# Optimization experiments

Hardware: AMD Instinct MI355X
Metric: run time of the kernel (lower is better)

The kernel has to match this reference:

```python
import jax, jax.numpy as jnp
import numpy as np

PD = 256            # pretrain_dim == dim_in (standard mode)
DZ = 128            # dim_z
PD2 = PD + 2        # feature dim after concatenating 2-d coords
FD = PD + 2 * PD2   # final_dim = 772
TEMP = float(DZ) ** 0.5
EPS = 1e-12
N1, N2 = 4096, 2048


def _lin_init(key, din, dout):
    w = jax.random.normal(key, (dout, din), jnp.float32) * 0.02
    b = jnp.zeros((dout,), jnp.float32)
    return w, b


def _lin(x, w, b):
    return x @ w.T + b


def setup_inputs() -> dict:
    key = jax.random.key(0)
    ks = jax.random.split(key, 13)
    lm_X = jax.random.normal(ks[0], (N1, PD), jnp.float32)
    lm_Y = jax.random.normal(ks[1], (N1, 2), jnp.float32)
    tg_X = jax.random.normal(ks[2], (N2, PD), jnp.float32)
    tg_Y = jax.random.normal(ks[3], (N2, 2), jnp.float32)
    lm_delay = jax.random.uniform(ks[4], (N1,), jnp.float32)
    tg_delay = jax.random.uniform(ks[5], (N2,), jnp.float32)
    aq_w, aq_b = _lin_init(ks[6], PD, DZ)    # att_attribute q proj
    ak_w, ak_b = _lin_init(ks[7], PD, DZ)    # att_attribute k proj
    w1_w, w1_b = _lin_init(ks[8], PD2, PD2)  # self.w_1
    w2_w, w2_b = _lin_init(ks[9], PD2, PD2)  # self.w_2
    pq_w, pq_b = _lin_init(ks[10], FD, DZ)   # pred attention q proj
    pk_w, pk_b = _lin_init(ks[11], PD, DZ)   # pred attention k proj
    pv_w, pv_b = _lin_init(ks[12], 2, 2)     # pred attention v proj
    gamma1 = jnp.ones((1, 1), jnp.float32)
    gamma2 = jnp.ones((1, 1), jnp.float32)
    gamma3 = jnp.ones((1, 1), jnp.float32)
    alpha = jnp.ones((1, 1), jnp.float32)
    beta = jnp.zeros((1, 1), jnp.float32)
    return dict(lm_X=lm_X, lm_Y=lm_Y, tg_X=tg_X, tg_Y=tg_Y,
                lm_delay=lm_delay, tg_delay=tg_delay,
                aq_w=aq_w, aq_b=aq_b, ak_w=ak_w, ak_b=ak_b,
                w1_w=w1_w, w1_b=w1_b, w2_w=w2_w, w2_b=w2_b,
                pq_w=pq_w, pq_b=pq_b, pk_w=pk_w, pk_b=pk_b,
                pv_w=pv_w, pv_b=pv_b,
                gamma1=gamma1, gamma2=gamma2, gamma3=gamma3,
                alpha=alpha, beta=beta)


def reference(lm_X, lm_Y, tg_X, tg_Y, lm_delay, tg_delay,
              aq_w, aq_b, ak_w, ak_b,
              w1_w, w1_b, w2_w, w2_b,
              pq_w, pq_b, pk_w, pk_b, pv_w, pv_b,
              gamma1, gamma2, gamma3, alpha, beta):
    n2 = tg_X.shape[0]
    a = alpha[0, 0]
    b0 = beta[0, 0]

    lm_feature = jnp.concatenate([lm_X, lm_Y], axis=1)            # [N1, PD2]
    tg_feature_0 = jnp.concatenate([tg_X, jnp.zeros((n2, 2), lm_X.dtype)], axis=1)
    router_0 = jnp.mean(lm_feature, axis=0)                        # [PD2]

    delay_score = jnp.exp(-gamma1[0, 0] * (a * lm_delay + b0))     # [N1]
    rou0 = jnp.exp(-gamma2[0, 0] * (a * tg_delay + b0))            # [N2]
    rou1 = jnp.exp(-gamma3[0, 0] * (a * tg_delay + b0))            # [N2]

    # SimpleAttention1: attribute score of targets over landmarks
    q = _lin(tg_X, aq_w, aq_b)
    k = _lin(lm_X, ak_w, ak_b)
    attr = jnp.exp(jax.nn.softmax((q / TEMP) @ k.T, axis=-1))      # [N2, N1]

    # Degree-normalized propagation of adj_matrix_0 (block-structured:
    # lm rows = identity, tg rows = [attr | I | rou0-col], router row = [delay | 0 | 1]).
    deg_tg0 = 1.0 + attr.sum(axis=1) + rou0                        # [N2]
    tg_prop0 = (attr @ lm_feature + tg_feature_0 + rou0[:, None] * router_0[None, :]) \
               / (deg_tg0 + EPS)[:, None]
    router_prop0 = (delay_score @ lm_feature + router_0) / (1.0 + delay_score.sum() + EPS)

    tg_feature_1 = _lin(tg_prop0, w1_w, w1_b)                      # [N2, PD2]
    router_1 = _lin(router_prop0[None, :], w1_w, w1_b)             # [1, PD2]

    # Second propagation: adj_matrix_1 = I + rou1 on tg->router column.
    tg_prop1 = (tg_feature_1 + rou1[:, None] * router_1) / (1.0 + rou1 + EPS)[:, None]
    tg_feature_2 = _lin(tg_prop1, w2_w, w2_b)                      # [N2, PD2]

    final_tg_feature = jnp.concatenate([tg_X, tg_feature_1, tg_feature_2], axis=-1)  # [N2, FD]

    # SimpleAttention2 (collaborative MLP prediction)
    q2 = _lin(final_tg_feature, pq_w, pq_b)
    k2 = _lin(lm_X, pk_w, pk_b)
    v2 = _lin(lm_Y, pv_w, pv_b)
    attn2 = jax.nn.softmax((q2 / TEMP) @ k2.T, axis=-1)            # [N2, N1]
    y_pred = attn2 @ v2                                            # [N2, 2]
    return y_pred, final_tg_feature
```

## Files before the change

### kernel.cpp

```cpp
#include <hip/hip_runtime.h>

#define N1 4096
#define N2 2048
#define PD 256
#define DZ 128
#define PD2 258
#define PD2P 264
#define FD 772
#define FDP 776
#define APN 272
#define APLD 72
#define SPLITS 16

typedef short s8v __attribute__((ext_vector_type(8)));
typedef float f32x4 __attribute__((ext_vector_type(4)));

__device__ __forceinline__ short f2b(float f) {
    union { float f; unsigned u; } v; v.f = f;
    unsigned r = v.u + 0x7fffu + ((v.u >> 16) & 1u);
    return (short)(r >> 16);
}
__device__ __forceinline__ float sb2f(short s) {
    union { unsigned u; float f; } v;
    v.u = ((unsigned)(unsigned short)s) << 16;
    return v.f;
}

constexpr int S0 = N1 * PD;
constexpr int S1 = S0 + N2 * PD;
constexpr int S2 = S1 + DZ * PD;
constexpr int S3 = S2 + 256 * 256;
constexpr int S4 = S3 + DZ * FDP;
constexpr int S5 = S4 + PD2 * PD2P;
constexpr int S6 = S5 + PD2 * PD2P;
constexpr int S7 = S6 + APN * N1;
constexpr int S8 = S7 + N1;
constexpr int S9 = S8 + 2048 + 8192 + 12288 + 256;

__global__ __launch_bounds__(256) void cvt_all(
    const float* __restrict__ lmX, const float* __restrict__ lmY,
    const float* __restrict__ tgX,
    const float* __restrict__ aqw, const float* __restrict__ akw,
    const float* __restrict__ pkw, const float* __restrict__ pqw,
    const float* __restrict__ w1w, const float* __restrict__ w2w,
    const float* __restrict__ lmd, const float* __restrict__ tgd,
    const float* __restrict__ g1, const float* __restrict__ g2,
    const float* __restrict__ g3, const float* __restrict__ al,
    const float* __restrict__ be,
    const float* __restrict__ pvw, const float* __restrict__ pvb,
    const float* __restrict__ akb, const float* __restrict__ pkb,
    short* __restrict__ lmXb, short* __restrict__ tgXb,
    short* __restrict__ aqwb, short* __restrict__ wkkb,
    short* __restrict__ pqwb,
    short* __restrict__ w1wb, short* __restrict__ w2wb,
    short* __restrict__ lmFTb,
    float* __restrict__ dscore, float* __restrict__ rou0,
    float* __restrict__ rou1, float* __restrict__ v2b,
    float* __restrict__ Z, short* __restrict__ finalFb,
    short* __restrict__ tgp1b, float* __restrict__ biasKK,
    float* __restrict__ outF)
{
    int i = blockIdx.x * 256 + threadIdx.x;
    if (i < S0) { lmXb[i] = f2b(lmX[i]); return; }
    if (i < S1) { int j = i - S0; int r = j >> 8, c = j & 255;
                  float v = tgX[j];
                  tgXb[j] = f2b(v);
                  outF[(size_t)r * FD + c] = v;
                  finalFb[(size_t)r * FDP + c] = f2b(v); return; }
    if (i < S2) { int j = i - S1; aqwb[j] = f2b(aqw[j]); return; }
    if (i < S3) { int j = i - S2; int r = j >> 8, c = j & 255;
                  wkkb[j] = f2b(r < 128 ? akw[r * 256 + c] : pkw[(r - 128) * 256 + c]);
                  return; }
    if (i < S4) { int j = i - S3; int r = j / FDP, c = j - r * FDP;
                  pqwb[j] = (c < FD) ? f2b(pqw[r * FD + c]) : (short)0; return; }
    if (i < S5) { int j = i - S4; int r = j / PD2P, c = j - r * PD2P;
                  w1wb[j] = (c < PD2) ? f2b(w1w[r * PD2 + c]) : (short)0; return; }
    if (i < S6) { int j = i - S5; int r = j / PD2P, c = j - r * PD2P;
                  w2wb[j] = (c < PD2) ? f2b(w2w[r * PD2 + c]) : (short)0; return; }
    if (i < S7) { int j = i - S6; int c = j >> 12, r = j & (N1 - 1);
                  float v = 0.f;
                  if (c < PD) v = lmX[r * PD + c];
                  else if (c < PD2) v = lmY[r * 2 + (c - PD)];
                  else if (c == PD2) v = 1.0f;
                  lmFTb[j] = f2b(v); return; }
    if (i < S8) { int j = i - S7;
                  float a = al[0], b = be[0];
                  dscore[j] = __expf(-g1[0] * (a * lmd[j] + b));
                  float y0 = lmY[2 * j], y1 = lmY[2 * j + 1];
                  v2b[2 * j]     = pvw[0] * y0 + pvw[1] * y1 + pvb[0];
                  v2b[2 * j + 1] = pvw[2] * y0 + pvw[3] * y1 + pvb[1];
                  if (j < N2) { float t = a * tgd[j] + b;
                                rou0[j] = __expf(-g2[0] * t);
                                rou1[j] = __expf(-g3[0] * t); }
                  return; }
    if (i < S9) { int j = i - S8;
                  if (j < 2048) { Z[j] = 0.f; return; }
                  j -= 2048;
                  if (j < 8192) { int r = j >> 2, c = FD + (j & 3);
                                  finalFb[(size_t)r * FDP + c] = 0; return; }
                  j -= 8192;
                  if (j < 12288) { int r = j / 6, c = PD2 + (j - r * 6);
                                   tgp1b[(size_t)r * PD2P + c] = 0; return; }
                  j -= 12288;
                  biasKK[j] = (j < 128) ? akb[j] : pkb[j - 128];
                  return; }
}

__global__ __launch_bounds__(256) void router_kernel(const short* __restrict__ lmFTb,
                                                     const float* __restrict__ dscore,
                                                     float* __restrict__ router0,
                                                     float* __restrict__ routerp0) {
    int c = blockIdx.x;
    const short* rowp = lmFTb + (size_t)c * N1;
    __shared__ float r1[256], r2[256], r3[256];
    int tid = threadIdx.x;
    float s1 = 0.f, s2 = 0.f, s3 = 0.f;
    for (int i = tid; i < N1; i += 256) {
        float v = sb2f(rowp[i]);
        float d = dscore[i];
        s1 += v; s2 += d * v; s3 += d;
    }
    r1[tid] = s1; r2[tid] = s2; r3[tid] = s3; __syncthreads();
    for (int o = 128; o > 0; o >>= 1) {
        if (tid < o) { r1[tid] += r1[tid + o]; r2[tid] += r2[tid + o]; r3[tid] += r3[tid + o]; }
        __syncthreads();
    }
    if (tid == 0) {
        float r0 = r1[0] / (float)N1;
        router0[c] = r0;
        routerp0[c] = (r2[0] + r0) / (1.f + r3[0] + 1e-12f);
    }
}

__global__ __launch_bounds__(256) void router1_kernel(const float* __restrict__ rp0,
                                                      const float* __restrict__ w1w,
                                                      const float* __restrict__ w1b,
                                                      float* __restrict__ router1) {
    for (int c = threadIdx.x; c < PD2; c += 256) {
        float s = w1b[c];
        const float* wr = w1w + (size_t)c * PD2;
        for (int k = 0; k < PD2; ++k) s += rp0[k] * wr[k];
        router1[c] = s;
    }
}

__global__ __launch_bounds__(256) void proj_gemm(
    const short* __restrict__ A, const short* __restrict__ B,
    const float* __restrict__ bias, short* __restrict__ outB,
    int M, int N, int KP, int ldo, float scale)
{
    __shared__ short Als[64][40];
    __shared__ short Bls[64][40];
    const int tid = threadIdx.x;
    const int wave = tid >> 6, lane = tid & 63;
    const int wm = wave >> 1, wn = wave & 1;
    const int lm = lane & 15, lq = lane >> 4;
    const int row0 = blockIdx.y * 64, col0 = blockIdx.x * 64;
    f32x4 acc[2][2];
    const f32x4 zero4 = {0.f, 0.f, 0.f, 0.f};
#pragma unroll
    for (int mt = 0; mt < 2; ++mt)
#pragma unroll
        for (int nt = 0; nt < 2; ++nt) acc[mt][nt] = zero4;
    const s8v zero8 = {0, 0, 0, 0, 0, 0, 0, 0};
    for (int k0 = 0; k0 < KP; k0 += 32) {
        {
            int r = tid >> 2, cg = tid & 3;
            int gk = k0 + cg * 8;
            s8v va = zero8, vb = zero8;
            if (row0 + r < M && gk < KP) va = *(const s8v*)(A + (size_t)(row0 + r) * KP + gk);
            if (col0 + r < N && gk < KP) vb = *(const s8v*)(B + (size_t)(col0 + r) * KP + gk);
            *(s8v*)(&Als[r][cg * 8]) = va;
            *(s8v*)(&Bls[r][cg * 8]) = vb;
        }
        __syncthreads();
        s8v af[2], bf[2];
#pragma unroll
        for (int mt = 0; mt < 2; ++mt)
            af[mt] = *(const s8v*)(&Als[wm * 32 + mt * 16 + lm][lq * 8]);
#pragma unroll
        for (int nt = 0; nt < 2; ++nt)
            bf[nt] = *(const s8v*)(&Bls[wn * 32 + nt * 16 + lm][lq * 8]);
#pragma unroll
        for (int mt = 0; mt < 2; ++mt)
#pragma unroll
            for (int nt = 0; nt < 2; ++nt)
                acc[mt][nt] = __builtin_amdgcn_mfma_f32_16x16x32_bf16(
                    af[mt], bf[nt], acc[mt][nt], 0, 0, 0);
        __syncthreads();
    }
#pragma unroll
    for (int mt = 0; mt < 2; ++mt)
#pragma unroll
        for (int nt = 0; nt < 2; ++nt) {
            int c = col0 + wn * 32 + nt * 16 + lm;
            if (c >= N) continue;
            float bv = bias ? bias[c] : 0.f;
#pragma unroll
            for (int i = 0; i < 4; ++i) {
                int r = row0 + wm * 32 + mt * 16 + lq * 4 + i;
                if (r >= M) continue;
                outB[(size_t)r * ldo + c] = f2b(scale * (acc[mt][nt][i] + bv));
            }
        }
}

__global__ __launch_bounds__(256) void scores_e(
    const short* __restrict__ Q,
    const short* __restrict__ Kk,
    short* __restrict__ E, float* __restrict__ Z)
{
    __shared__ short Als[128][40];
    __shared__ short Bls[128][40];
    const int tid = threadIdx.x;
    const int wave = tid >> 6, lane = tid & 63;
    const int wm = wave >> 1, wn = wave & 1;
    const int lm = lane & 15, lq = lane >> 4;
    const int row0 = blockIdx.y * 128, col0 = blockIdx.x * 128;
    f32x4 acc[4][4];
    const f32x4 zero4 = {0.f, 0.f, 0.f, 0.f};
#pragma unroll
    for (int mt = 0; mt < 4; ++mt)
#pragma unroll
        for (int nt = 0; nt < 4; ++nt) acc[mt][nt] = zero4;
    for (int k0 = 0; k0 < 128; k0 += 32) {
#pragma unroll
        for (int l = 0; l < 2; ++l) {
            int id = l * 256 + tid;
            int r = id >> 2, cg = id & 3;
            int gk = k0 + cg * 8;
            *(s8v*)(&Als[r][cg * 8]) = *(const s8v*)(Q + (size_t)(row0 + r) * DZ + gk);
            *(s8v*)(&Bls[r][cg * 8]) = *(const s8v*)(Kk + (size_t)(col0 + r) * 256 + gk);
        }
        __syncthreads();
        s8v af[4], bf[4];
#pragma unroll
        for (int mt = 0; mt < 4; ++mt)
            af[mt] = *(const s8v*)(&Als[wm * 64 + mt * 16 + lm][lq * 8]);
#pragma unroll
        for (int nt = 0; nt < 4; ++nt)
            bf[nt] = *(const s8v*)(&Bls[wn * 64 + nt * 16 + lm][lq * 8]);
#pragma unroll
        for (int mt = 0; mt < 4; ++mt)
#pragma unroll
            for (int nt = 0; nt < 4; ++nt)
                acc[mt][nt] = __builtin_amdgcn_mfma_f32_16x16x32_bf16(
                    af[mt], bf[nt], acc[mt][nt], 0, 0, 0);
        __syncthreads();
    }
#pragma unroll
    for (int mt = 0; mt < 4; ++mt)
#pragma unroll
        for (int i = 0; i < 4; ++i) {
            int r = row0 + wm * 64 + mt * 16 + lq * 4 + i;
            float rs = 0.f;
#pragma unroll
            for (int nt = 0; nt < 4; ++nt) {
                int c = col0 + wn * 64 + nt * 16 + lm;
                float e = __expf(acc[mt][nt][i]);
                E[(size_t)r * N1 + c] = f2b(e);
                rs += e;
            }
#pragma unroll
            for (int msk = 1; msk < 16; msk <<= 1) rs += __shfl_xor(rs, msk, 64);
            if (lm == 0) atomicAdd(&Z[r], rs);
        }
}

__global__ __launch_bounds__(256) void ap_gemm(const short* __restrict__ E,
                                               const float* __restrict__ Z,
                                               const short* __restrict__ lmFTb,
                                               float* __restrict__ part)
{
    __shared__ short Als[128 * APLD];
    __shared__ short Bls[APN * APLD];
    const int tid = threadIdx.x;
    const int wave = tid >> 6, lane = tid & 63;
    const int lm = lane & 15, lq = lane >> 4;
    const int s = blockIdx.x;
    const int row0 = blockIdx.y * 128;
    const int kbase = s * (N1 / SPLITS);
    f32x4 acc0[17], acc1[17];
    const f32x4 zero4 = {0.f, 0.f, 0.f, 0.f};
#pragma unroll
    for (int nt = 0; nt < 17; ++nt) { acc0[nt] = zero4; acc1[nt] = zero4; }

    for (int it = 0; it < (N1 / SPLITS) / 64; ++it) {
        int k0 = kbase + it * 64;
#pragma unroll
        for (int l = 0; l < 4; ++l) {
            int id = l * 256 + tid;
            int r = id >> 3, g = id & 7;
            s8v ev = *(const s8v*)(E + (size_t)(row0 + r) * N1 + k0 + g * 8);
            float invZ = __builtin_amdgcn_rcpf(Z[row0 + r]);
            s8v av;
#pragma unroll
            for (int j = 0; j < 8; ++j)
                av[j] = f2b(__expf(sb2f(ev[j]) * invZ));
            *(s8v*)(&Als[r * APLD + g * 8]) = av;
        }
#pragma unroll
        for (int l = 0; l < 9; ++l) {
            int id = l * 256 + tid;
            if (id < APN * 8) {
                int r = id >> 3, g = id & 7;
                *(s8v*)(&Bls[r * APLD + g * 8]) =
                    *(const s8v*)(lmFTb + (size_t)r * N1 + k0 + g * 8);
            }
        }
        __syncthreads();
        s8v a00 = *(const s8v*)(&Als[(wave * 32 + lm) * APLD + lq * 8]);
        s8v a01 = *(const s8v*)(&Als[(wave * 32 + lm) * APLD + 32 + lq * 8]);
        s8v a10 = *(const s8v*)(&Als[(wave * 32 + 16 + lm) * APLD + lq * 8]);
        s8v a11 = *(const s8v*)(&Als[(wave * 32 + 16 + lm) * APLD + 32 + lq * 8]);
#pragma unroll
        for (int nt = 0; nt < 17; ++nt) {
            s8v b0 = *(const s8v*)(&Bls[(nt * 16 + lm) * APLD + lq * 8]);
            s8v b1 = *(const s8v*)(&Bls[(nt * 16 + lm) * APLD + 32 + lq * 8]);
            acc0[nt] = __builtin_amdgcn_mfma_f32_16x16x32_bf16(a00, b0, acc0[nt], 0, 0, 0);
            acc0[nt] = __builtin_amdgcn_mfma_f32_16x16x32_bf16(a01, b1, acc0[nt], 0, 0, 0);
            acc1[nt] = __builtin_amdgcn_mfma_f32_16x16x32_bf16(a10, b0, acc1[nt], 0, 0, 0);
            acc1[nt] = __builtin_amdgcn_mfma_f32_16x16x32_bf16(a11, b1, acc1[nt], 0, 0, 0);
        }
        __syncthreads();
    }
    float* op = part + (size_t)s * N2 * APN;
#pragma unroll
    for (int nt = 0; nt < 17; ++nt) {
        int c = nt * 16 + lm;
#pragma unroll
        for (int i = 0; i < 4; ++i) {
            int r = row0 + wave * 32 + lq * 4 + i;
            op[(size_t)r * APN + c] = acc0[nt][i];
            op[(size_t)(r + 16) * APN + c] = acc1[nt][i];
        }
    }
}

__global__ __launch_bounds__(256) void fix_tgp0(const float* __restrict__ part,
                                                const float* __restrict__ tgX,
                                                const float* __restrict__ rou0,
                                                const float* __restrict__ router0,
                                                short* __restrict__ outb) {
    int r = blockIdx.x;
    int tid = threadIdx.x;
    __shared__ float sAsum;
    float s0 = 0.f, s1 = 0.f;
#pragma unroll
    for (int s = 0; s < SPLITS; ++s)
        s0 += part[((size_t)s * N2 + r) * APN + tid];
    if (tid < 8) {
#pragma unroll
        for (int s = 0; s < SPLITS; ++s)
            s1 += part[((size_t)s * N2 + r) * APN + 256 + tid];
    }
    if (tid == 2) sAsum = s1;
    __syncthreads();
    float ro = rou0[r];
    float inv = 1.f / (1.f + sAsum + ro + 1e-12f);
    {
        float v = (s0 + tgX[(size_t)r * PD + tid] + ro * router0[tid]) * inv;
        outb[(size_t)r * PD2P + tid] = f2b(v);
    }
    if (tid < 8) {
        int c = 256 + tid;
        float v = 0.f;
        if (c < PD2) v = (s1 + ro * router0[c]) * inv;
        outb[(size_t)r * PD2P + c] = f2b(v);
    }
}

__global__ __launch_bounds__(256) void w_gemm(
    const short* __restrict__ A, const short* __restrict__ B,
    const float* __restrict__ bias,
    float* __restrict__ outFcol, short* __restrict__ fFbcol,
    const float* __restrict__ rou1, const float* __restrict__ router1,
    short* __restrict__ tgp1b)
{
    __shared__ short Als[64][40];
    __shared__ short Bls[64][40];
    const int tid = threadIdx.x;
    const int wave = tid >> 6, lane = tid & 63;
    const int wm = wave >> 1, wn = wave & 1;
    const int lm = lane & 15, lq = lane >> 4;
    const int row0 = blockIdx.y * 64, col0 = blockIdx.x * 64;
    f32x4 acc[2][2];
    const f32x4 zero4 = {0.f, 0.f, 0.f, 0.f};
#pragma unroll
    for (int mt = 0; mt < 2; ++mt)
#pragma unroll
        for (int nt = 0; nt < 2; ++nt) acc[mt][nt] = zero4;
    const s8v zero8 = {0, 0, 0, 0, 0, 0, 0, 0};
    for (int k0 = 0; k0 < PD2P; k0 += 32) {
        {
            int r = tid >> 2, cg = tid & 3;
            int gk = k0 + cg * 8;
            s8v va = zero8, vb = zero8;
            if (gk < PD2P) {
                va = *(const s8v*)(A + (size_t)(row0 + r) * PD2P + gk);
                if (col0 + r < PD2) vb = *(const s8v*)(B + (size_t)(col0 + r) * PD2P + gk);
            }
            *(s8v*)(&Als[r][cg * 8]) = va;
            *(s8v*)(&Bls[r][cg * 8]) = vb;
        }
        __syncthreads();
        s8v af[2], bf[2];
#pragma unroll
        for (int mt = 0; mt < 2; ++mt)
            af[mt] = *(const s8v*)(&Als[wm * 32 + mt * 16 + lm][lq * 8]);
#pragma unroll
        for (int nt = 0; nt < 2; ++nt)
            bf[nt] = *(const s8v*)(&Bls[wn * 32 + nt * 16 + lm][lq * 8]);
#pragma unroll
        for (int mt = 0; mt < 2; ++mt)
#pragma unroll
            for (int nt = 0; nt < 2; ++nt)
                acc[mt][nt] = __builtin_amdgcn_mfma_f32_16x16x32_bf16(
                    af[mt], bf[nt], acc[mt][nt], 0, 0, 0);
        __syncthreads();
    }
#pragma unroll
    for (int mt = 0; mt < 2; ++mt)
#pragma unroll
        for (int nt = 0; nt < 2; ++nt) {
            int c = col0 + wn * 32 + nt * 16 + lm;
            if (c >= PD2) continue;
            float bv = bias[c];
            float rc = router1 ? router1[c] : 0.f;
#pragma unroll
            for (int i = 0; i < 4; ++i) {
                int r = row0 + wm * 32 + mt * 16 + lq * 4 + i;
                float v = acc[mt][nt][i] + bv;
                outFcol[(size_t)r * FD + c] = v;
                fFbcol[(size_t)r * FDP + c] = f2b(v);
                if (tgp1b) {
                    float ro = rou1[r];
                    float t = (v + ro * rc) / (1.f + ro + 1e-12f);
                    tgp1b[(size_t)r * PD2P + c] = f2b(t);
                }
            }
        }
}

__global__ __launch_bounds__(256) void attn2_flash(
    const short* __restrict__ Q,
    const short* __restrict__ Kk,
    const float* __restrict__ V, float* __restrict__ part2)
{
    __shared__ short Qls[64 * 136];
    __shared__ short Kls[64 * 136];
    __shared__ float Vls[128];
    const int tid = threadIdx.x;
    const int wave = tid >> 6, lane = tid & 63;
    const int lm = lane & 15, lq = lane >> 4;
    const int chunk = blockIdx.x;
    const int row0 = blockIdx.y * 64;
#pragma unroll
    for (int l = 0; l < 4; ++l) {
        int id = l * 256 + tid;
        int r = id >> 4, g = id & 15;
        *(s8v*)(&Qls[r * 136 + g * 8]) = *(const s8v*)(Q + (size_t)(row0 + r) * DZ + g * 8);
    }
    __syncthreads();
    s8v af[4];
#pragma unroll
    for (int ks = 0; ks < 4; ++ks)
        af[ks] = *(const s8v*)(&Qls[(wave * 16 + lm) * 136 + ks * 32 + lq * 8]);
    float z[4] = {0.f, 0.f, 0.f, 0.f}, y0[4] = {0.f, 0.f, 0.f, 0.f}, y1[4] = {0.f, 0.f, 0.f, 0.f};

    for (int t = 0; t < 8; ++t) {
        int col0 = chunk * 512 + t * 64;
        __syncthreads();
#pragma unroll
        for (int l = 0; l < 4; ++l) {
            int id = l * 256 + tid;
            int r = id >> 4, g = id & 15;
            *(s8v*)(&Kls[r * 136 + g * 8]) =
                *(const s8v*)(Kk + (size_t)(col0 + r) * 256 + 128 + g * 8);
        }
        if (tid < 128) Vls[tid] = V[col0 * 2 + tid];
        __syncthreads();
        f32x4 acc[4];
        const f32x4 zero4 = {0.f, 0.f, 0.f, 0.f};
#pragma unroll
        for (int nt = 0; nt < 4; ++nt) acc[nt] = zero4;
#pragma unroll
        for (int nt = 0; nt < 4; ++nt)
#pragma unroll
            for (int ks = 0; ks < 4; ++ks) {
                s8v bf = *(const s8v*)(&Kls[(nt * 16 + lm) * 136 + ks * 32 + lq * 8]);
                acc[nt] = __builtin_amdgcn_mfma_f32_16x16x32_bf16(af[ks], bf, acc[nt], 0, 0, 0);
            }
        float v0[4], v1[4];
#pragma unroll
        for (int nt = 0; nt < 4; ++nt) {
            v0[nt] = Vls[(nt * 16 + lm) * 2];
            v1[nt] = Vls[(nt * 16 + lm) * 2 + 1];
        }
#pragma unroll
        for (int i = 0; i < 4; ++i) {
            float e0 = __expf(acc[0][i]), e1 = __expf(acc[1][i]);
            float e2 = __expf(acc[2][i]), e3 = __expf(acc[3][i]);
            float pz = e0 + e1 + e2 + e3;
            float py0 = e0 * v0[0] + e1 * v0[1] + e2 * v0[2] + e3 * v0[3];
            float py1 = e0 * v1[0] + e1 * v1[1] + e2 * v1[2] + e3 * v1[3];
#pragma unroll
            for (int msk = 1; msk < 16; msk <<= 1) {
                pz  += __shfl_xor(pz, msk, 64);
                py0 += __shfl_xor(py0, msk, 64);
                py1 += __shfl_xor(py1, msk, 64);
            }
            z[i] += pz; y0[i] += py0; y1[i] += py1;
        }
    }
    if (lm == 0) {
#pragma unroll
        for (int i = 0; i < 4; ++i) {
            int r = row0 + wave * 16 + lq * 4 + i;
            float* p = part2 + ((size_t)r * 8 + chunk) * 4;
            p[0] = z[i]; p[1] = y0[i]; p[2] = y1[i];
        }
    }
}

__global__ void attn2_combine(const float* __restrict__ part2, float* __restrict__ out) {
    int r = blockIdx.x * blockDim.x + threadIdx.x;
    if (r >= N2) return;
    const float* p = part2 + (size_t)r * 32;
    float Zt = 0.f, Y0 = 0.f, Y1 = 0.f;
#pragma unroll
    for (int c = 0; c < 8; ++c) {
        Zt += p[c * 4]; Y0 += p[c * 4 + 1]; Y1 += p[c * 4 + 2];
    }
    out[2 * r] = Y0 / Zt;
    out[2 * r + 1] = Y1 / Zt;
}

extern "C" void kernel_launch(void* const* d_in, const int* in_sizes, int n_in,
                              void* d_out, int out_size, void* d_ws, size_t ws_size,
                              hipStream_t stream) {
    const float* lm_X = (const float*)d_in[0];
    const float* lm_Y = (const float*)d_in[1];
    const float* tg_X = (const float*)d_in[2];
    const float* lm_delay = (const float*)d_in[4];
    const float* tg_delay = (const float*)d_in[5];
    const float* aq_w = (const float*)d_in[6];
    const float* aq_b = (const float*)d_in[7];
    const float* ak_w = (const float*)d_in[8];
    const float* ak_b = (const float*)d_in[9];
    const float* w1_w = (const float*)d_in[10];
    const float* w1_b = (const float*)d_in[11];
    const float* w2_w = (const float*)d_in[12];
    const float* w2_b = (const float*)d_in[13];
    const float* pq_w = (const float*)d_in[14];
    const float* pq_b = (const float*)d_in[15];
    const float* pk_w = (const float*)d_in[16];
    const float* pk_b = (const float*)d_in[17];
    const float* pv_w = (const float*)d_in[18];
    const float* pv_b = (const float*)d_in[19];
    const float* g1 = (const float*)d_in[20];
    const float* g2 = (const float*)d_in[21];
    const float* g3 = (const float*)d_in[22];
    const float* al = (const float*)d_in[23];
    const float* be = (const float*)d_in[24];

    float* out = (float*)d_out;
    float* outF = out + (size_t)N2 * 2;

    char* base = (char*)d_ws;
    size_t off = 0;
    auto allocF = [&](size_t n) -> float* {
        float* p = (float*)(base + off);
        off += (n * 4 + 255) / 256 * 256;
        return p;
    };
    auto allocS = [&](size_t n) -> short* {
        short* p = (short*)(base + off);
        off += (n * 2 + 255) / 256 * 256;
        return p;
    };

    short* E        = allocS((size_t)N2 * N1);
    float* appart   = allocF((size_t)SPLITS * N2 * APN);
    short* lmFTb    = allocS((size_t)APN * N1);
    short* lmXb     = allocS((size_t)N1 * PD);
    short* tgXb     = allocS((size_t)N2 * PD);
    short* qb_b     = allocS((size_t)N2 * DZ);
    short* kk       = allocS((size_t)N1 * 256);
    short* q2_b     = allocS((size_t)N2 * DZ);
    short* tgp0b    = allocS((size_t)N2 * PD2P);
    short* tgp1b    = allocS((size_t)N2 * PD2P);
    short* finalFb  = allocS((size_t)N2 * FDP);
    short* aqwb     = allocS((size_t)DZ * PD);
    short* wkkb     = allocS((size_t)256 * 256);
    short* pqwb     = allocS((size_t)DZ * FDP);
    short* w1wb     = allocS((size_t)PD2 * PD2P);
    short* w2wb     = allocS((size_t)PD2 * PD2P);
    float* v2b      = allocF((size_t)N1 * 2);
    float* part2    = allocF((size_t)N2 * 32);
    float* Zbuf     = allocF(N2);
    float* biasKK   = allocF(256);
    float* router0  = allocF(PD2);
    float* routerp0 = allocF(PD2);
    float* router1  = allocF(PD2);
    float* dscore   = allocF(N1);
    float* rou0     = allocF(N2);
    float* rou1     = allocF(N2);

    const float INV_TEMP = 0.08838834764831845f;

    hipLaunchKernelGGL(cvt_all, dim3((S9 + 255) / 256), dim3(256), 0, stream,
                       lm_X, lm_Y, tg_X, aq_w, ak_w, pk_w, pq_w, w1_w, w2_w,
                       lm_delay, tg_delay, g1, g2, g3, al, be, pv_w, pv_b, ak_b, pk_b,
                       lmXb, tgXb, aqwb, wkkb, pqwb, w1wb, w2wb, lmFTb,
                       dscore, rou0, rou1, v2b, Zbuf, finalFb, tgp1b, biasKK, outF);
    hipLaunchKernelGGL(router_kernel, dim3(PD2), dim3(256), 0, stream,
                       lmFTb, dscore, router0, routerp0);
    hipLaunchKernelGGL(router1_kernel, dim3(1), dim3(256), 0, stream,
                       routerp0, w1_w, w1_b, router1);

    hipLaunchKernelGGL(proj_gemm, dim3(4, 64), dim3(256), 0, stream,
                       lmXb, wkkb, biasKK, kk, N1, 256, PD, 256, 1.f);
    hipLaunchKernelGGL(proj_gemm, dim3(2, 32), dim3(256), 0, stream,
                       tgXb, aqwb, aq_b, qb_b, N2, DZ, PD, DZ, INV_TEMP);
    hipLaunchKernelGGL(scores_e, dim3(32, 16), dim3(256), 0, stream, qb_b, kk, E, Zbuf);
    hipLaunchKernelGGL(ap_gemm, dim3(SPLITS, N2 / 128), dim3(256), 0, stream,
                       E, Zbuf, lmFTb, appart);
    hipLaunchKernelGGL(fix_tgp0, dim3(N2), dim3(256), 0, stream,
                       appart, tg_X, rou0, router0, tgp0b);
    hipLaunchKernelGGL(w_gemm, dim3(5, 32), dim3(256), 0, stream,
                       tgp0b, w1wb, w1_b, outF + 256, finalFb + 256, rou1, router1, tgp1b);
    hipLaunchKernelGGL(w_gemm, dim3(5, 32), dim3(256), 0, stream,
                       tgp1b, w2wb, w2_b, outF + 514, finalFb + 514,
                       nullptr, nullptr, nullptr);
    hipLaunchKernelGGL(proj_gemm, dim3(2, 32), dim3(256), 0, stream,
                       finalFb, pqwb, pq_b, q2_b, N2, DZ, FDP, DZ, INV_TEMP);
    hipLaunchKernelGGL(attn2_flash, dim3(8, N2 / 64), dim3(256), 0, stream,
                       q2_b, kk, v2b, part2);
    hipLaunchKernelGGL(attn2_combine, dim3((N2 + 255) / 256), dim3(256), 0, stream,
                       part2, out);
}
```

Measured before the change: 252.2 us.

## Fuse all stages into one persistent megakernel with grid-wide barriers

```diff
diff --git a/kernel.cpp b/kernel.cpp
--- a/kernel.cpp
+++ b/kernel.cpp
@@ -26,617 +26,626 @@
     return v.f;
 }
 
-constexpr int S0 = N1 * PD;
-constexpr int S1 = S0 + N2 * PD;
-constexpr int S2 = S1 + DZ * PD;
-constexpr int S3 = S2 + 256 * 256;
-constexpr int S4 = S3 + DZ * FDP;
-constexpr int S5 = S4 + PD2 * PD2P;
-constexpr int S6 = S5 + PD2 * PD2P;
-constexpr int S7 = S6 + APN * N1;
-constexpr int S8 = S7 + N1;
-constexpr int S9 = S8 + 2048 + 8192 + 12288 + 256;
-
-__global__ __launch_bounds__(256) void cvt_all(
-    const float* __restrict__ lmX, const float* __restrict__ lmY,
-    const float* __restrict__ tgX,
-    const float* __restrict__ aqw, const float* __restrict__ akw,
-    const float* __restrict__ pkw, const float* __restrict__ pqw,
-    const float* __restrict__ w1w, const float* __restrict__ w2w,
-    const float* __restrict__ lmd, const float* __restrict__ tgd,
-    const float* __restrict__ g1, const float* __restrict__ g2,
-    const float* __restrict__ g3, const float* __restrict__ al,
-    const float* __restrict__ be,
-    const float* __restrict__ pvw, const float* __restrict__ pvb,
-    const float* __restrict__ akb, const float* __restrict__ pkb,
-    short* __restrict__ lmXb, short* __restrict__ tgXb,
-    short* __restrict__ aqwb, short* __restrict__ wkkb,
-    short* __restrict__ pqwb,
-    short* __restrict__ w1wb, short* __restrict__ w2wb,
-    short* __restrict__ lmFTb,
-    float* __restrict__ dscore, float* __restrict__ rou0,
-    float* __restrict__ rou1, float* __restrict__ v2b,
-    float* __restrict__ Z, short* __restrict__ finalFb,
-    short* __restrict__ tgp1b, float* __restrict__ biasKK,
-    float* __restrict__ outF)
-{
-    int i = blockIdx.x * 256 + threadIdx.x;
-    if (i < S0) { lmXb[i] = f2b(lmX[i]); return; }
-    if (i < S1) { int j = i - S0; int r = j >> 8, c = j & 255;
-                  float v = tgX[j];
-                  tgXb[j] = f2b(v);
-                  outF[(size_t)r * FD + c] = v;
-                  finalFb[(size_t)r * FDP + c] = f2b(v); return; }
-    if (i < S2) { int j = i - S1; aqwb[j] = f2b(aqw[j]); return; }
-    if (i < S3) { int j = i - S2; int r = j >> 8, c = j & 255;
-                  wkkb[j] = f2b(r < 128 ? akw[r * 256 + c] : pkw[(r - 128) * 256 + c]);
-                  return; }
-    if (i < S4) { int j = i - S3; int r = j / FDP, c = j - r * FDP;
-                  pqwb[j] = (c < FD) ? f2b(pqw[r * FD + c]) : (short)0; return; }
-    if (i < S5) { int j = i - S4; int r = j / PD2P, c = j - r * PD2P;
-                  w1wb[j] = (c < PD2) ? f2b(w1w[r * PD2 + c]) : (short)0; return; }
-    if (i < S6) { int j = i - S5; int r = j / PD2P, c = j - r * PD2P;
-                  w2wb[j] = (c < PD2) ? f2b(w2w[r * PD2 + c]) : (short)0; return; }
-    if (i < S7) { int j = i - S6; int c = j >> 12, r = j & (N1 - 1);
-                  float v = 0.f;
-                  if (c < PD) v = lmX[r * PD + c];
-                  else if (c < PD2) v = lmY[r * 2 + (c - PD)];
-                  else if (c == PD2) v = 1.0f;
-                  lmFTb[j] = f2b(v); return; }
-    if (i < S8) { int j = i - S7;
-                  float a = al[0], b = be[0];
-                  dscore[j] = __expf(-g1[0] * (a * lmd[j] + b));
-                  float y0 = lmY[2 * j], y1 = lmY[2 * j + 1];
-                  v2b[2 * j]     = pvw[0] * y0 + pvw[1] * y1 + pvb[0];
-                  v2b[2 * j + 1] = pvw[2] * y0 + pvw[3] * y1 + pvb[1];
-                  if (j < N2) { float t = a * tgd[j] + b;
-                                rou0[j] = __expf(-g2[0] * t);
-                                rou1[j] = __expf(-g3[0] * t); }
-                  return; }
-    if (i < S9) { int j = i - S8;
-                  if (j < 2048) { Z[j] = 0.f; return; }
-                  j -= 2048;
-                  if (j < 8192) { int r = j >> 2, c = FD + (j & 3);
-                                  finalFb[(size_t)r * FDP + c] = 0; return; }
-                  j -= 8192;
-                  if (j < 12288) { int r = j / 6, c = PD2 + (j - r * 6);
-                                   tgp1b[(size_t)r * PD2P + c] = 0; return; }
-                  j -= 12288;
-                  biasKK[j] = (j < 128) ? akb[j] : pkb[j - 128];
-                  return; }
+struct P {
+    const float *lmX, *lmY, *tgX, *lmd, *tgd;
+    const float *aqw, *aqb, *akw, *akb, *w1w, *w1b, *w2w, *w2b;
+    const float *pqw, *pqb, *pkw, *pkb, *pvw, *pvb;
+    const float *g1, *g2, *g3, *al, *be;
+    short *lmFTb, *qb, *kk, *q2, *tgp0b, *tgp1b, *finalFb, *w1wb, *w2wb, *pqwb, *E;
+    float *appart, *v2b, *part2, *Z;
+    float *router0, *routerp0, *router1, *dscore, *rou0, *rou1;
+    float *out, *outF;
+    unsigned *bar;
+};
+
+__device__ __forceinline__ void gbar(unsigned* cnt, unsigned target) {
+    __syncthreads();
+    if (threadIdx.x == 0) {
+        __threadfence();
+        atomicAdd(cnt, 1u);
+        while (__hip_atomic_load(cnt, __ATOMIC_RELAXED, __HIP_MEMORY_SCOPE_AGENT) < target)
+            __builtin_amdgcn_s_sleep(2);
+        __threadfence();
+    }
+    __syncthreads();
 }
 
-__global__ __launch_bounds__(256) void router_kernel(const short* __restrict__ lmFTb,
-                                                     const float* __restrict__ dscore,
-                                                     float* __restrict__ router0,
-                                                     float* __restrict__ routerp0) {
-    int c = blockIdx.x;
-    const short* rowp = lmFTb + (size_t)c * N1;
-    __shared__ float r1[256], r2[256], r3[256];
-    int tid = threadIdx.x;
-    float s1 = 0.f, s2 = 0.f, s3 = 0.f;
-    for (int i = tid; i < N1; i += 256) {
-        float v = sb2f(rowp[i]);
-        float d = dscore[i];
-        s1 += v; s2 += d * v; s3 += d;
-    }
-    r1[tid] = s1; r2[tid] = s2; r3[tid] = s3; __syncthreads();
-    for (int o = 128; o > 0; o >>= 1) {
-        if (tid < o) { r1[tid] += r1[tid + o]; r2[tid] += r2[tid + o]; r3[tid] += r3[tid + o]; }
-        __syncthreads();
-    }
-    if (tid == 0) {
-        float r0 = r1[0] / (float)N1;
-        router0[c] = r0;
-        routerp0[c] = (r2[0] + r0) / (1.f + r3[0] + 1e-12f);
-    }
+#define F_TGX   (N2 * PD)
+#define F_W     (PD2 * PD2P)
+#define F_PQ    (DZ * FDP)
+#define F_DEL   4096
+#define F_Z     2048
+#define F_FPAD  (N2 * 4)
+#define F_TPAD  (N2 * 6)
+#define FT_TOT  (F_TGX + 2 * F_W + F_PQ + F_DEL + F_Z + F_FPAD + F_TPAD)
+
+__device__ __forceinline__ void mfma64(const short* Als, const short* Bls,
+                                       f32x4 acc[2][2], int wm, int wn, int lm, int lq) {
+    s8v af[2], bf[2];
+#pragma unroll
+    for (int mt = 0; mt < 2; ++mt)
+        af[mt] = *(const s8v*)(Als + (wm * 32 + mt * 16 + lm) * 40 + lq * 8);
+#pragma unroll
+    for (int nt = 0; nt < 2; ++nt)
+        bf[nt] = *(const s8v*)(Bls + (wn * 32 + nt * 16 + lm) * 40 + lq * 8);
+#pragma unroll
+    for (int mt = 0; mt < 2; ++mt)
+#pragma unroll
+        for (int nt = 0; nt < 2; ++nt)
+            acc[mt][nt] = __builtin_amdgcn_mfma_f32_16x16x32_bf16(
+                af[mt], bf[nt], acc[mt][nt], 0, 0, 0);
 }
 
-__global__ __launch_bounds__(256) void router1_kernel(const float* __restrict__ rp0,
-                                                      const float* __restrict__ w1w,
-                                                      const float* __restrict__ w1b,
-                                                      float* __restrict__ router1) {
-    for (int c = threadIdx.x; c < PD2; c += 256) {
-        float s = w1b[c];
-        const float* wr = w1w + (size_t)c * PD2;
-        for (int k = 0; k < PD2; ++k) s += rp0[k] * wr[k];
-        router1[c] = s;
-    }
-}
-
-__global__ __launch_bounds__(256) void proj_gemm(
-    const short* __restrict__ A, const short* __restrict__ B,
-    const float* __restrict__ bias, short* __restrict__ outB,
-    int M, int N, int KP, int ldo, float scale)
-{
-    __shared__ short Als[64][40];
-    __shared__ short Bls[64][40];
-    const int tid = threadIdx.x;
+__global__ __launch_bounds__(256) void mega(P p) {
+    __shared__ __align__(16) short LDS[28800];
+    const int bid = blockIdx.x, tid = threadIdx.x;
     const int wave = tid >> 6, lane = tid & 63;
     const int wm = wave >> 1, wn = wave & 1;
     const int lm = lane & 15, lq = lane >> 4;
-    const int row0 = blockIdx.y * 64, col0 = blockIdx.x * 64;
-    f32x4 acc[2][2];
     const f32x4 zero4 = {0.f, 0.f, 0.f, 0.f};
-#pragma unroll
-    for (int mt = 0; mt < 2; ++mt)
-#pragma unroll
-        for (int nt = 0; nt < 2; ++nt) acc[mt][nt] = zero4;
-    const s8v zero8 = {0, 0, 0, 0, 0, 0, 0, 0};
-    for (int k0 = 0; k0 < KP; k0 += 32) {
-        {
-            int r = tid >> 2, cg = tid & 3;
-            int gk = k0 + cg * 8;
+
+    for (int j = bid; j < 320; j += 256) {
+        int rt = j / 5, ct = j - rt * 5;
+        int r0 = rt * 64, c0 = ct * 64;
+        __syncthreads();
+#pragma unroll
+        for (int l = 0; l < 16; ++l) {
+            int idx = l * 256 + tid;
+            int i = idx >> 6, jj = idx & 63;
+            int c = c0 + jj;
+            float v = 0.f;
+            if (c < PD) v = p.lmX[(size_t)(r0 + i) * PD + c];
+            else if (c < PD2) v = p.lmY[(size_t)(r0 + i) * 2 + (c - PD)];
+            else if (c == PD2) v = 1.f;
+            LDS[jj * 65 + i] = f2b(v);
+        }
+        __syncthreads();
+#pragma unroll
+        for (int l = 0; l < 16; ++l) {
+            int idx = l * 256 + tid;
+            int cc = idx >> 6, i = idx & 63;
+            if (c0 + cc < APN)
+                p.lmFTb[(size_t)(c0 + cc) * N1 + r0 + i] = LDS[cc * 65 + i];
+        }
+    }
+    for (int i0 = bid * 256 + tid; i0 < FT_TOT; i0 += 65536) {
+        int j = i0;
+        if (j < F_TGX) {
+            int r = j >> 8, c = j & 255;
+            float v = p.tgX[j];
+            p.outF[(size_t)r * FD + c] = v;
+            p.finalFb[(size_t)r * FDP + c] = f2b(v);
+            continue;
+        }
+        j -= F_TGX;
+        if (j < F_W) { int r = j / PD2P, c = j - r * PD2P;
+            p.w1wb[j] = (c < PD2) ? f2b(p.w1w[r * PD2 + c]) : (short)0; continue; }
+        j -= F_W;
+        if (j < F_W) { int r = j / PD2P, c = j - r * PD2P;
+            p.w2wb[j] = (c < PD2) ? f2b(p.w2w[r * PD2 + c]) : (short)0; continue; }
+        j -= F_W;
+        if (j < F_PQ) { int r = j / FDP, c = j - r * FDP;
+            p.pqwb[j] = (c < FD) ? f2b(p.pqw[r * FD + c]) : (short)0; continue; }
+        j -= F_PQ;
+        if (j < F_DEL) {
+            float a = p.al[0], b = p.be[0];
+            p.dscore[j] = __expf(-p.g1[0] * (a * p.lmd[j] + b));
+            float y0 = p.lmY[2 * j], y1 = p.lmY[2 * j + 1];
+            p.v2b[2 * j]     = p.pvw[0] * y0 + p.pvw[1] * y1 + p.pvb[0];
+            p.v2b[2 * j + 1] = p.pvw[2] * y0 + p.pvw[3] * y1 + p.pvb[1];
+            if (j < N2) {
+                float t = a * p.tgd[j] + b;
+                p.rou0[j] = __expf(-p.g2[0] * t);
+                p.rou1[j] = __expf(-p.g3[0] * t);
+            }
+            continue;
+        }
+        j -= F_DEL;
+        if (j < F_Z) { p.Z[j] = 0.f; continue; }
+        j -= F_Z;
+        if (j < F_FPAD) { int r = j >> 2;
+            p.finalFb[(size_t)r * FDP + FD + (j & 3)] = 0; continue; }
+        j -= F_FPAD;
+        { int r = j / 6; p.tgp1b[(size_t)r * PD2P + PD2 + (j - r * 6)] = 0; }
+    }
+    gbar(p.bar, 256u * 1);
+
+    for (int j = bid; j < 578; j += 256) {
+        __syncthreads();
+        if (j < 258) {
+            float* r1 = (float*)LDS;
+            float* r2 = r1 + 256;
+            float* r3 = r2 + 256;
+            const short* rowp = p.lmFTb + (size_t)j * N1;
+            float s1 = 0.f, s2 = 0.f, s3 = 0.f;
+            for (int i = tid; i < N1; i += 256) {
+                float v = sb2f(rowp[i]);
+                float d = p.dscore[i];
+                s1 += v; s2 += d * v; s3 += d;
+            }
+            r1[tid] = s1; r2[tid] = s2; r3[tid] = s3; __syncthreads();
+            for (int o = 128; o > 0; o >>= 1) {
+                if (tid < o) { r1[tid] += r1[tid + o]; r2[tid] += r2[tid + o]; r3[tid] += r3[tid + o]; }
+                __syncthreads();
+            }
+            if (tid == 0) {
+                float r0v = r1[0] / (float)N1;
+                p.router0[j] = r0v;
+                p.routerp0[j] = (r2[0] + r0v) / (1.f + r3[0] + 1e-12f);
+            }
+        } else if (j < 514) {
+            int jt = j - 258;
+            int row0 = (jt >> 2) * 64, col0 = (jt & 3) * 64;
+            short* Als = LDS;
+            short* Bls = LDS + 64 * 40;
+            f32x4 acc[2][2] = {{zero4, zero4}, {zero4, zero4}};
+            int r = tid >> 2, cgp = tid & 3;
+            for (int k0 = 0; k0 < 256; k0 += 32) {
+                int gk = k0 + cgp * 8;
+                const float* ap = p.lmX + (size_t)(row0 + r) * PD + gk;
+                int c = col0 + r;
+                const float* bp = (c < 128) ? p.akw + (size_t)c * PD + gk
+                                            : p.pkw + (size_t)(c - 128) * PD + gk;
+                s8v va, vb;
+#pragma unroll
+                for (int q = 0; q < 8; ++q) { va[q] = f2b(ap[q]); vb[q] = f2b(bp[q]); }
+                *(s8v*)(Als + r * 40 + cgp * 8) = va;
+                *(s8v*)(Bls + r * 40 + cgp * 8) = vb;
+                __syncthreads();
+                mfma64(Als, Bls, acc, wm, wn, lm, lq);
+                __syncthreads();
+            }
+#pragma unroll
+            for (int mt = 0; mt < 2; ++mt)
+#pragma unroll
+                for (int nt = 0; nt < 2; ++nt) {
+                    int c = col0 + wn * 32 + nt * 16 + lm;
+                    float bv = (c < 128) ? p.akb[c] : p.pkb[c - 128];
+#pragma unroll
+                    for (int i = 0; i < 4; ++i) {
+                        int rr = row0 + wm * 32 + mt * 16 + lq * 4 + i;
+                        p.kk[(size_t)rr * 256 + c] = f2b(acc[mt][nt][i] + bv);
+                    }
+                }
+        } else {
+            int jt = j - 514;
+            int row0 = (jt >> 1) * 64, col0 = (jt & 1) * 64;
+            short* Als = LDS;
+            short* Bls = LDS + 64 * 40;
+            f32x4 acc[2][2] = {{zero4, zero4}, {zero4, zero4}};
+            int r = tid >> 2, cgp = tid & 3;
+            for (int k0 = 0; k0 < 256; k0 += 32) {
+                int gk = k0 + cgp * 8;
+                const float* ap = p.tgX + (size_t)(row0 + r) * PD + gk;
+                const float* bp = p.aqw + (size_t)(col0 + r) * PD + gk;
+                s8v va, vb;
+#pragma unroll
+                for (int q = 0; q < 8; ++q) { va[q] = f2b(ap[q]); vb[q] = f2b(bp[q]); }
+                *(s8v*)(Als + r * 40 + cgp * 8) = va;
+                *(s8v*)(Bls + r * 40 + cgp * 8) = vb;
+                __syncthreads();
+                mfma64(Als, Bls, acc, wm, wn, lm, lq);
+                __syncthreads();
+            }
+            const float INV_TEMP = 0.08838834764831845f;
+#pragma unroll
+            for (int mt = 0; mt < 2; ++mt)
+#pragma unroll
+                for (int nt = 0; nt < 2; ++nt) {
+                    int c = col0 + wn * 32 + nt * 16 + lm;
+                    float bv = p.aqb[c];
+#pragma unroll
+                    for (int i = 0; i < 4; ++i) {
+                        int rr = row0 + wm * 32 + mt * 16 + lq * 4 + i;
+                        p.qb[(size_t)rr * DZ + c] = f2b(INV_TEMP * (acc[mt][nt][i] + bv));
+                    }
+                }
+        }
+    }
+    gbar(p.bar, 256u * 2);
+
+    for (int j = bid; j < 513; j += 256) {
+        __syncthreads();
+        if (j < 512) {
+            int row0 = (j >> 5) * 128, col0 = (j & 31) * 128;
+            short* Als = LDS;
+            short* Bls = LDS + 128 * 40;
+            f32x4 acc[4][4];
+#pragma unroll
+            for (int mt = 0; mt < 4; ++mt)
+#pragma unroll
+                for (int nt = 0; nt < 4; ++nt) acc[mt][nt] = zero4;
+            for (int k0 = 0; k0 < 128; k0 += 32) {
+#pragma unroll
+                for (int l = 0; l < 2; ++l) {
+                    int id = l * 256 + tid;
+                    int r = id >> 2, cgp = id & 3;
+                    int gk = k0 + cgp * 8;
+                    *(s8v*)(Als + r * 40 + cgp * 8) =
+                        *(const s8v*)(p.qb + (size_t)(row0 + r) * DZ + gk);
+                    *(s8v*)(Bls + r * 40 + cgp * 8) =
+                        *(const s8v*)(p.kk + (size_t)(col0 + r) * 256 + gk);
+                }
+                __syncthreads();
+                s8v af[4], bf[4];
+#pragma unroll
+                for (int mt = 0; mt < 4; ++mt)
+                    af[mt] = *(const s8v*)(Als + (wm * 64 + mt * 16 + lm) * 40 + lq * 8);
+#pragma unroll
+                for (int nt = 0; nt < 4; ++nt)
+                    bf[nt] = *(const s8v*)(Bls + (wn * 64 + nt * 16 + lm) * 40 + lq * 8);
+#pragma unroll
+                for (int mt = 0; mt < 4; ++mt)
+#pragma unroll
+                    for (int nt = 0; nt < 4; ++nt)
+                        acc[mt][nt] = __builtin_amdgcn_mfma_f32_16x16x32_bf16(
+                            af[mt], bf[nt], acc[mt][nt], 0, 0, 0);
+                __syncthreads();
+            }
+#pragma unroll
+            for (int mt = 0; mt < 4; ++mt)
+#pragma unroll
+                for (int i = 0; i < 4; ++i) {
+                    int r = row0 + wm * 64 + mt * 16 + lq * 4 + i;
+                    float rs = 0.f;
+#pragma unroll
+                    for (int nt = 0; nt < 4; ++nt) {
+                        int c = col0 + wn * 64 + nt * 16 + lm;
+                        float e = __expf(acc[mt][nt][i]);
+                        p.E[(size_t)r * N1 + c] = f2b(e);
+                        rs += e;
+                    }
+#pragma unroll
+                    for (int msk = 1; msk < 16; msk <<= 1) rs += __shfl_xor(rs, msk, 64);
+                    if (lm == 0) atomicAdd(&p.Z[r], rs);
+                }
+        } else {
+            for (int c = tid; c < PD2; c += 256) {
+                float s = p.w1b[c];
+                const float* wr = p.w1w + (size_t)c * PD2;
+                for (int k = 0; k < PD2; ++k) s += p.routerp0[k] * wr[k];
+                p.router1[c] = s;
+            }
+        }
+    }
+    gbar(p.bar, 256u * 3);
+
+    {
+        int s = bid & 15, row0 = (bid >> 4) * 128;
+        int kbase = s * (N1 / SPLITS);
+        short* Als = LDS;
+        short* Bls = LDS + 128 * APLD;
+        f32x4 acc0[17], acc1[17];
+#pragma unroll
+        for (int nt = 0; nt < 17; ++nt) { acc0[nt] = zero4; acc1[nt] = zero4; }
+        for (int it = 0; it < (N1 / SPLITS) / 64; ++it) {
+            int k0 = kbase + it * 64;
+#pragma unroll
+            for (int l = 0; l < 4; ++l) {
+                int id = l * 256 + tid;
+                int r = id >> 3, g = id & 7;
+                s8v ev = *(const s8v*)(p.E + (size_t)(row0 + r) * N1 + k0 + g * 8);
+                float invZ = __builtin_amdgcn_rcpf(p.Z[row0 + r]);
+                s8v av;
+#pragma unroll
+                for (int q = 0; q < 8; ++q)
+                    av[q] = f2b(__expf(sb2f(ev[q]) * invZ));
+                *(s8v*)(Als + r * APLD + g * 8) = av;
+            }
+#pragma unroll
+            for (int l = 0; l < 9; ++l) {
+                int id = l * 256 + tid;
+                if (id < APN * 8) {
+                    int r = id >> 3, g = id & 7;
+                    *(s8v*)(Bls + r * APLD + g * 8) =
+                        *(const s8v*)(p.lmFTb + (size_t)r * N1 + k0 + g * 8);
+                }
+            }
+            __syncthreads();
+            s8v a00 = *(const s8v*)(Als + (wave * 32 + lm) * APLD + lq * 8);
+            s8v a01 = *(const s8v*)(Als + (wave * 32 + lm) * APLD + 32 + lq * 8);
+            s8v a10 = *(const s8v*)(Als + (wave * 32 + 16 + lm) * APLD + lq * 8);
+            s8v a11 = *(const s8v*)(Als + (wave * 32 + 16 + lm) * APLD + 32 + lq * 8);
+#pragma unroll
+            for (int nt = 0; nt < 17; ++nt) {
+                s8v b0 = *(const s8v*)(Bls + (nt * 16 + lm) * APLD + lq * 8);
+                s8v b1 = *(const s8v*)(Bls + (nt * 16 + lm) * APLD + 32 + lq * 8);
+                acc0[nt] = __builtin_amdgcn_mfma_f32_16x16x32_bf16(a00, b0, acc0[nt], 0, 0, 0);
+                acc0[nt] = __builtin_amdgcn_mfma_f32_16x16x32_bf16(a01, b1, acc0[nt], 0, 0, 0);
+                acc1[nt] = __builtin_amdgcn_mfma_f32_16x16x32_bf16(a10, b0, acc1[nt], 0, 0, 0);
+                acc1[nt] = __builtin_amdgcn_mfma_f32_16x16x32_bf16(a11, b1, acc1[nt], 0, 0, 0);
+            }
+            __syncthreads();
+        }
+        float* op = p.appart + (size_t)s * N2 * APN;
+#pragma unroll
+        for (int nt = 0; nt < 17; ++nt) {
+            int c = nt * 16 + lm;
+#pragma unroll
+            for (int i = 0; i < 4; ++i) {
+                int r = row0 + wave * 32 + lq * 4 + i;
+                op[(size_t)r * APN + c] = acc0[nt][i];
+                op[(size_t)(r + 16) * APN + c] = acc1[nt][i];
+            }
+        }
+    }
+    gbar(p.bar, 256u * 4);
+
+    for (int rr = 0; rr < 8; ++rr) {
+        int r = bid * 8 + rr;
+        float s0 = 0.f, s1 = 0.f;
+#pragma unroll
+        for (int s = 0; s < SPLITS; ++s)
+            s0 += p.appart[((size_t)s * N2 + r) * APN + tid];
+        if (tid < 8) {
+#pragma unroll
+            for (int s = 0; s < SPLITS; ++s)
+                s1 += p.appart[((size_t)s * N2 + r) * APN + 256 + tid];
+        }
+        __syncthreads();
+        if (tid == 2) *(float*)LDS = s1;
+        __syncthreads();
+        float asum = *(float*)LDS;
+        float ro = p.rou0[r];
+        float inv = 1.f / (1.f + asum + ro + 1e-12f);
+        float v = (s0 + p.tgX[(size_t)r * PD + tid] + ro * p.router0[tid]) * inv;
+        p.tgp0b[(size_t)r * PD2P + tid] = f2b(v);
+        if (tid < 8) {
+            int c = 256 + tid;
+            float v2 = 0.f;
+            if (c < PD2) v2 = (s1 + ro * p.router0[c]) * inv;
+            p.tgp0b[(size_t)r * PD2P + c] = f2b(v2);
+        }
+        __syncthreads();
+    }
+    gbar(p.bar, 256u * 5);
+
+    for (int layer = 0; layer < 2; ++layer) {
+        const short* A = layer ? p.tgp1b : p.tgp0b;
+        const short* B = layer ? p.w2wb : p.w1wb;
+        const float* bias = layer ? p.w2b : p.w1b;
+        float* oF = p.outF + (layer ? 514 : 256);
+        short* oB = p.finalFb + (layer ? 514 : 256);
+        for (int j = bid; j < 160; j += 256) {
+            int row0 = (j / 5) * 64, col0 = (j % 5) * 64;
+            short* Als = LDS;
+            short* Bls = LDS + 64 * 40;
+            f32x4 acc[2][2] = {{zero4, zero4}, {zero4, zero4}};
+            const s8v zero8 = {0, 0, 0, 0, 0, 0, 0, 0};
+            int r = tid >> 2, cgp = tid & 3;
+            for (int k0 = 0; k0 < PD2P; k0 += 32) {
+                int gk = k0 + cgp * 8;
+                s8v va = zero8, vb = zero8;
+                if (gk < PD2P) {
+                    va = *(const s8v*)(A + (size_t)(row0 + r) * PD2P + gk);
+                    if (col0 + r < PD2) vb = *(const s8v*)(B + (size_t)(col0 + r) * PD2P + gk);
+                }
+                *(s8v*)(Als + r * 40 + cgp * 8) = va;
+                *(s8v*)(Bls + r * 40 + cgp * 8) = vb;
+                __syncthreads();
+                mfma64(Als, Bls, acc, wm, wn, lm, lq);
+                __syncthreads();
+            }
+#pragma unroll
+            for (int mt = 0; mt < 2; ++mt)
+#pragma unroll
+                for (int nt = 0; nt < 2; ++nt) {
+                    int c = col0 + wn * 32 + nt * 16 + lm;
+                    if (c >= PD2) continue;
+                    float bv = bias[c];
+                    float rc = p.router1[c];
+#pragma unroll
+                    for (int i = 0; i < 4; ++i) {
+                        int rr = row0 + wm * 32 + mt * 16 + lq * 4 + i;
+                        float v = acc[mt][nt][i] + bv;
+                        oF[(size_t)rr * FD + c] = v;
+                        oB[(size_t)rr * FDP + c] = f2b(v);
+                        if (layer == 0) {
+                            float ro = p.rou1[rr];
+                            p.tgp1b[(size_t)rr * PD2P + c] =
+                                f2b((v + ro * rc) / (1.f + ro + 1e-12f));
+                        }
+                    }
+                }
+        }
+        gbar(p.bar, 256u * (6 + layer));
+    }
+
+    for (int j = bid; j < 64; j += 256) {
+        int row0 = (j >> 1) * 64, col0 = (j & 1) * 64;
+        short* Als = LDS;
+        short* Bls = LDS + 64 * 40;
+        f32x4 acc[2][2] = {{zero4, zero4}, {zero4, zero4}};
+        const s8v zero8 = {0, 0, 0, 0, 0, 0, 0, 0};
+        int r = tid >> 2, cgp = tid & 3;
+        for (int k0 = 0; k0 < FDP; k0 += 32) {
+            int gk = k0 + cgp * 8;
             s8v va = zero8, vb = zero8;
-            if (row0 + r < M && gk < KP) va = *(const s8v*)(A + (size_t)(row0 + r) * KP + gk);
-            if (col0 + r < N && gk < KP) vb = *(const s8v*)(B + (size_t)(col0 + r) * KP + gk);
-            *(s8v*)(&Als[r][cg * 8]) = va;
-            *(s8v*)(&Bls[r][cg * 8]) = vb;
-        }
-        __syncthreads();
-        s8v af[2], bf[2];
+            if (gk < FDP) {
+                va = *(const s8v*)(p.finalFb + (size_t)(row0 + r) * FDP + gk);
+                vb = *(const s8v*)(p.pqwb + (size_t)(col0 + r) * FDP + gk);
+            }
+            *(s8v*)(Als + r * 40 + cgp * 8) = va;
+            *(s8v*)(Bls + r * 40 + cgp * 8) = vb;
+            __syncthreads();
+            mfma64(Als, Bls, acc, wm, wn, lm, lq);
+            __syncthreads();
+        }
+        const float INV_TEMP = 0.08838834764831845f;
 #pragma unroll
         for (int mt = 0; mt < 2; ++mt)
-            af[mt] = *(const s8v*)(&Als[wm * 32 + mt * 16 + lm][lq * 8]);
-#pragma unroll
-        for (int nt = 0; nt < 2; ++nt)
-            bf[nt] = *(const s8v*)(&Bls[wn * 32 + nt * 16 + lm][lq * 8]);
-#pragma unroll
-        for (int mt = 0; mt < 2; ++mt)
-#pragma unroll
-            for (int nt = 0; nt < 2; ++nt)
-                acc[mt][nt] = __builtin_amdgcn_mfma_f32_16x16x32_bf16(
-                    af[mt], bf[nt], acc[mt][nt], 0, 0, 0);
-        __syncthreads();
-    }
-#pragma unroll
-    for (int mt = 0; mt < 2; ++mt)
-#pragma unroll
-        for (int nt = 0; nt < 2; ++nt) {
-            int c = col0 + wn * 32 + nt * 16 + lm;
-            if (c >= N) continue;
-            float bv = bias ? bias[c] : 0.f;
-#pragma unroll
-            for (int i = 0; i < 4; ++i) {
-                int r = row0 + wm * 32 + mt * 16 + lq * 4 + i;
-                if (r >= M) continue;
-                outB[(size_t)r * ldo + c] = f2b(scale * (acc[mt][nt][i] + bv));
-            }
-        }
-}
-
-__global__ __launch_bounds__(256) void scores_e(
-    const short* __restrict__ Q,
-    const short* __restrict__ Kk,
-    short* __restrict__ E, float* __restrict__ Z)
-{
-    __shared__ short Als[128][40];
-    __shared__ short Bls[128][40];
-    const int tid = threadIdx.x;
-    const int wave = tid >> 6, lane = tid & 63;
-    const int wm = wave >> 1, wn = wave & 1;
-    const int lm = lane & 15, lq = lane >> 4;
-    const int row0 = blockIdx.y * 128, col0 = blockIdx.x * 128;
-    f32x4 acc[4][4];
-    const f32x4 zero4 = {0.f, 0.f, 0.f, 0.f};
-#pragma unroll
-    for (int mt = 0; mt < 4; ++mt)
-#pragma unroll
-        for (int nt = 0; nt < 4; ++nt) acc[mt][nt] = zero4;
-    for (int k0 = 0; k0 < 128; k0 += 32) {
-#pragma unroll
-        for (int l = 0; l < 2; ++l) {
-            int id = l * 256 + tid;
-            int r = id >> 2, cg = id & 3;
-            int gk = k0 + cg * 8;
-            *(s8v*)(&Als[r][cg * 8]) = *(const s8v*)(Q + (size_t)(row0 + r) * DZ + gk);
-            *(s8v*)(&Bls[r][cg * 8]) = *(const s8v*)(Kk + (size_t)(col0 + r) * 256 + gk);
-        }
-        __syncthreads();
-        s8v af[4], bf[4];
-#pragma unroll
-        for (int mt = 0; mt < 4; ++mt)
-            af[mt] = *(const s8v*)(&Als[wm * 64 + mt * 16 + lm][lq * 8]);
-#pragma unroll
-        for (int nt = 0; nt < 4; ++nt)
-            bf[nt] = *(const s8v*)(&Bls[wn * 64 + nt * 16 + lm][lq * 8]);
-#pragma unroll
-        for (int mt = 0; mt < 4; ++mt)
-#pragma unroll
-            for (int nt = 0; nt < 4; ++nt)
-                acc[mt][nt] = __builtin_amdgcn_mfma_f32_16x16x32_bf16(
-                    af[mt], bf[nt], acc[mt][nt], 0, 0, 0);
-        __syncthreads();
-    }
-#pragma unroll
-    for (int mt = 0; mt < 4; ++mt)
-#pragma unroll
-        for (int i = 0; i < 4; ++i) {
-            int r = row0 + wm * 64 + mt * 16 + lq * 4 + i;
-            float rs = 0.f;
-#pragma unroll
-            for (int nt = 0; nt < 4; ++nt) {
-                int c = col0 + wn * 64 + nt * 16 + lm;
-                float e = __expf(acc[mt][nt][i]);
-                E[(size_t)r * N1 + c] = f2b(e);
-                rs += e;
-            }
-#pragma unroll
-            for (int msk = 1; msk < 16; msk <<= 1) rs += __shfl_xor(rs, msk, 64);
-            if (lm == 0) atomicAdd(&Z[r], rs);
-        }
-}
-
-__global__ __launch_bounds__(256) void ap_gemm(const short* __restrict__ E,
-                                               const float* __restrict__ Z,
-                                               const short* __restrict__ lmFTb,
-                                               float* __restrict__ part)
-{
-    __shared__ short Als[128 * APLD];
-    __shared__ short Bls[APN * APLD];
-    const int tid = threadIdx.x;
-    const int wave = tid >> 6, lane = tid & 63;
-    const int lm = lane & 15, lq = lane >> 4;
-    const int s = blockIdx.x;
-    const int row0 = blockIdx.y * 128;
-    const int kbase = s * (N1 / SPLITS);
-    f32x4 acc0[17], acc1[17];
-    const f32x4 zero4 = {0.f, 0.f, 0.f, 0.f};
-#pragma unroll
-    for (int nt = 0; nt < 17; ++nt) { acc0[nt] = zero4; acc1[nt] = zero4; }
-
-    for (int it = 0; it < (N1 / SPLITS) / 64; ++it) {
-        int k0 = kbase + it * 64;
-#pragma unroll
-        for (int l = 0; l < 4; ++l) {
-            int id = l * 256 + tid;
-            int r = id >> 3, g = id & 7;
-            s8v ev = *(const s8v*)(E + (size_t)(row0 + r) * N1 + k0 + g * 8);
-            float invZ = __builtin_amdgcn_rcpf(Z[row0 + r]);
-            s8v av;
-#pragma unroll
-            for (int j = 0; j < 8; ++j)
-                av[j] = f2b(__expf(sb2f(ev[j]) * invZ));
-            *(s8v*)(&Als[r * APLD + g * 8]) = av;
-        }
-#pragma unroll
-        for (int l = 0; l < 9; ++l) {
-            int id = l * 256 + tid;
-            if (id < APN * 8) {
-                int r = id >> 3, g = id & 7;
-                *(s8v*)(&Bls[r * APLD + g * 8]) =
-                    *(const s8v*)(lmFTb + (size_t)r * N1 + k0 + g * 8);
-            }
-        }
-        __syncthreads();
-        s8v a00 = *(const s8v*)(&Als[(wave * 32 + lm) * APLD + lq * 8]);
-        s8v a01 = *(const s8v*)(&Als[(wave * 32 + lm) * APLD + 32 + lq * 8]);
-        s8v a10 = *(const s8v*)(&Als[(wave * 32 + 16 + lm) * APLD + lq * 8]);
-        s8v a11 = *(const s8v*)(&Als[(wave * 32 + 16 + lm) * APLD + 32 + lq * 8]);
-#pragma unroll
-        for (int nt = 0; nt < 17; ++nt) {
-            s8v b0 = *(const s8v*)(&Bls[(nt * 16 + lm) * APLD + lq * 8]);
-            s8v b1 = *(const s8v*)(&Bls[(nt * 16 + lm) * APLD + 32 + lq * 8]);
-            acc0[nt] = __builtin_amdgcn_mfma_f32_16x16x32_bf16(a00, b0, acc0[nt], 0, 0, 0);
-            acc0[nt] = __builtin_amdgcn_mfma_f32_16x16x32_bf16(a01, b1, acc0[nt], 0, 0, 0);
-            acc1[nt] = __builtin_amdgcn_mfma_f32_16x16x32_bf16(a10, b0, acc1[nt], 0, 0, 0);
-            acc1[nt] = __builtin_amdgcn_mfma_f32_16x16x32_bf16(a11, b1, acc1[nt], 0, 0, 0);
-        }
-        __syncthreads();
-    }
-    float* op = part + (size_t)s * N2 * APN;
-#pragma unroll
-    for (int nt = 0; nt < 17; ++nt) {
-        int c = nt * 16 + lm;
-#pragma unroll
-        for (int i = 0; i < 4; ++i) {
-            int r = row0 + wave * 32 + lq * 4 + i;
-            op[(size_t)r * APN + c] = acc0[nt][i];
-            op[(size_t)(r + 16) * APN + c] = acc1[nt][i];
-        }
-    }
-}
-
-__global__ __launch_bounds__(256) void fix_tgp0(const float* __restrict__ part,
-                                                const float* __restrict__ tgX,
-                                                const float* __restrict__ rou0,
-                                                const float* __restrict__ router0,
-                                                short* __restrict__ outb) {
-    int r = blockIdx.x;
-    int tid = threadIdx.x;
-    __shared__ float sAsum;
-    float s0 = 0.f, s1 = 0.f;
-#pragma unroll
-    for (int s = 0; s < SPLITS; ++s)
-        s0 += part[((size_t)s * N2 + r) * APN + tid];
-    if (tid < 8) {
-#pragma unroll
-        for (int s = 0; s < SPLITS; ++s)
-            s1 += part[((size_t)s * N2 + r) * APN + 256 + tid];
-    }
-    if (tid == 2) sAsum = s1;
-    __syncthreads();
-    float ro = rou0[r];
-    float inv = 1.f / (1.f + sAsum + ro + 1e-12f);
+#pragma unroll
+            for (int nt = 0; nt < 2; ++nt) {
+                int c = col0 + wn * 32 + nt * 16 + lm;
+                float bv = p.pqb[c];
+#pragma unroll
+                for (int i = 0; i < 4; ++i) {
+                    int rr = row0 + wm * 32 + mt * 16 + lq * 4 + i;
+                    p.q2[(size_t)rr * DZ + c] = f2b(INV_TEMP * (acc[mt][nt][i] + bv));
+                }
+            }
+    }
+    gbar(p.bar, 256u * 8);
+
     {
-        float v = (s0 + tgX[(size_t)r * PD + tid] + ro * router0[tid]) * inv;
-        outb[(size_t)r * PD2P + tid] = f2b(v);
-    }
-    if (tid < 8) {
-        int c = 256 + tid;
-        float v = 0.f;
-        if (c < PD2) v = (s1 + ro * router0[c]) * inv;
-        outb[(size_t)r * PD2P + c] = f2b(v);
-    }
-}
-
-__global__ __launch_bounds__(256) void w_gemm(
-    const short* __restrict__ A, const short* __restrict__ B,
-    const float* __restrict__ bias,
-    float* __restrict__ outFcol, short* __restrict__ fFbcol,
-    const float* __restrict__ rou1, const float* __restrict__ router1,
-    short* __restrict__ tgp1b)
-{
-    __shared__ short Als[64][40];
-    __shared__ short Bls[64][40];
-    const int tid = threadIdx.x;
-    const int wave = tid >> 6, lane = tid & 63;
-    const int wm = wave >> 1, wn = wave & 1;
-    const int lm = lane & 15, lq = lane >> 4;
-    const int row0 = blockIdx.y * 64, col0 = blockIdx.x * 64;
-    f32x4 acc[2][2];
-    const f32x4 zero4 = {0.f, 0.f, 0.f, 0.f};
-#pragma unroll
-    for (int mt = 0; mt < 2; ++mt)
-#pragma unroll
-        for (int nt = 0; nt < 2; ++nt) acc[mt][nt] = zero4;
-    const s8v zero8 = {0, 0, 0, 0, 0, 0, 0, 0};
-    for (int k0 = 0; k0 < PD2P; k0 += 32) {
-        {
-            int r = tid >> 2, cg = tid & 3;
-            int gk = k0 + cg * 8;
-            s8v va = zero8, vb = zero8;
-            if (gk < PD2P) {
-                va = *(const s8v*)(A + (size_t)(row0 + r) * PD2P + gk);
-                if (col0 + r < PD2) vb = *(const s8v*)(B + (size_t)(col0 + r) * PD2P + gk);
-            }
-            *(s8v*)(&Als[r][cg * 8]) = va;
-            *(s8v*)(&Bls[r][cg * 8]) = vb;
-        }
-        __syncthreads();
-        s8v af[2], bf[2];
-#pragma unroll
-        for (int mt = 0; mt < 2; ++mt)
-            af[mt] = *(const s8v*)(&Als[wm * 32 + mt * 16 + lm][lq * 8]);
-#pragma unroll
-        for (int nt = 0; nt < 2; ++nt)
-            bf[nt] = *(const s8v*)(&Bls[wn * 32 + nt * 16 + lm][lq * 8]);
-#pragma unroll
-        for (int mt = 0; mt < 2; ++mt)
-#pragma unroll
-            for (int nt = 0; nt < 2; ++nt)
-                acc[mt][nt] = __builtin_amdgcn_mfma_f32_16x16x32_bf16(
-                    af[mt], bf[nt], acc[mt][nt], 0, 0, 0);
-        __syncthreads();
-    }
-#pragma unroll
-    for (int mt = 0; mt < 2; ++mt)
-#pragma unroll
-        for (int nt = 0; nt < 2; ++nt) {
-            int c = col0 + wn * 32 + nt * 16 + lm;
-            if (c >= PD2) continue;
-            float bv = bias[c];
-            float rc = router1 ? router1[c] : 0.f;
-#pragma unroll
-            for (int i = 0; i < 4; ++i) {
-                int r = row0 + wm * 32 + mt * 16 + lq * 4 + i;
-                float v = acc[mt][nt][i] + bv;
-                outFcol[(size_t)r * FD + c] = v;
-                fFbcol[(size_t)r * FDP + c] = f2b(v);
-                if (tgp1b) {
-                    float ro = rou1[r];
-                    float t = (v + ro * rc) / (1.f + ro + 1e-12f);
-                    tgp1b[(size_t)r * PD2P + c] = f2b(t);
-                }
-            }
-        }
-}
-
-__global__ __launch_bounds__(256) void attn2_flash(
-    const short* __restrict__ Q,
-    const short* __restrict__ Kk,
-    const float* __restrict__ V, float* __restrict__ part2)
-{
-    __shared__ short Qls[64 * 136];
-    __shared__ short Kls[64 * 136];
-    __shared__ float Vls[128];
-    const int tid = threadIdx.x;
-    const int wave = tid >> 6, lane = tid & 63;
-    const int lm = lane & 15, lq = lane >> 4;
-    const int chunk = blockIdx.x;
-    const int row0 = blockIdx.y * 64;
-#pragma unroll
-    for (int l = 0; l < 4; ++l) {
-        int id = l * 256 + tid;
-        int r = id >> 4, g = id & 15;
-        *(s8v*)(&Qls[r * 136 + g * 8]) = *(const s8v*)(Q + (size_t)(row0 + r) * DZ + g * 8);
-    }
-    __syncthreads();
-    s8v af[4];
-#pragma unroll
-    for (int ks = 0; ks < 4; ++ks)
-        af[ks] = *(const s8v*)(&Qls[(wave * 16 + lm) * 136 + ks * 32 + lq * 8]);
-    float z[4] = {0.f, 0.f, 0.f, 0.f}, y0[4] = {0.f, 0.f, 0.f, 0.f}, y1[4] = {0.f, 0.f, 0.f, 0.f};
-
-    for (int t = 0; t < 8; ++t) {
-        int col0 = chunk * 512 + t * 64;
+        int chunk = bid & 7, row0 = (bid >> 3) * 64;
+        short* Qls = LDS;
+        short* Kls = LDS + 64 * 136;
+        float* Vls = (float*)(LDS + 2 * 64 * 136);
         __syncthreads();
 #pragma unroll
         for (int l = 0; l < 4; ++l) {
             int id = l * 256 + tid;
             int r = id >> 4, g = id & 15;
-            *(s8v*)(&Kls[r * 136 + g * 8]) =
-                *(const s8v*)(Kk + (size_t)(col0 + r) * 256 + 128 + g * 8);
-        }
-        if (tid < 128) Vls[tid] = V[col0 * 2 + tid];
-        __syncthreads();
-        f32x4 acc[4];
-        const f32x4 zero4 = {0.f, 0.f, 0.f, 0.f};
-#pragma unroll
-        for (int nt = 0; nt < 4; ++nt) acc[nt] = zero4;
-#pragma unroll
-        for (int nt = 0; nt < 4; ++nt)
-#pragma unroll
-            for (int ks = 0; ks < 4; ++ks) {
-                s8v bf = *(const s8v*)(&Kls[(nt * 16 + lm) * 136 + ks * 32 + lq * 8]);
-                acc[nt] = __builtin_amdgcn_mfma_f32_16x16x32_bf16(af[ks], bf, acc[nt], 0, 0, 0);
-            }
-        float v0[4], v1[4];
-#pragma unroll
-        for (int nt = 0; nt < 4; ++nt) {
-            v0[nt] = Vls[(nt * 16 + lm) * 2];
-            v1[nt] = Vls[(nt * 16 + lm) * 2 + 1];
-        }
-#pragma unroll
-        for (int i = 0; i < 4; ++i) {
-            float e0 = __expf(acc[0][i]), e1 = __expf(acc[1][i]);
-            float e2 = __expf(acc[2][i]), e3 = __expf(acc[3][i]);
-            float pz = e0 + e1 + e2 + e3;
-            float py0 = e0 * v0[0] + e1 * v0[1] + e2 * v0[2] + e3 * v0[3];
-            float py1 = e0 * v1[0] + e1 * v1[1] + e2 * v1[2] + e3 * v1[3];
-#pragma unroll
-            for (int msk = 1; msk < 16; msk <<= 1) {
-                pz  += __shfl_xor(pz, msk, 64);
-                py0 += __shfl_xor(py0, msk, 64);
-                py1 += __shfl_xor(py1, msk, 64);
-            }
-            z[i] += pz; y0[i] += py0; y1[i] += py1;
-        }
-    }
-    if (lm == 0) {
-#pragma unroll
-        for (int i = 0; i < 4; ++i) {
-            int r = row0 + wave * 16 + lq * 4 + i;
-            float* p = part2 + ((size_t)r * 8 + chunk) * 4;
-            p[0] = z[i]; p[1] = y0[i]; p[2] = y1[i];
-        }
-    }
-}
-
-__global__ void attn2_combine(const float* __restrict__ part2, float* __restrict__ out) {
-    int r = blockIdx.x * blockDim.x + threadIdx.x;
-    if (r >= N2) return;
-    const float* p = part2 + (size_t)r * 32;
-    float Zt = 0.f, Y0 = 0.f, Y1 = 0.f;
-#pragma unroll
-    for (int c = 0; c < 8; ++c) {
-        Zt += p[c * 4]; Y0 += p[c * 4 + 1]; Y1 += p[c * 4 + 2];
-    }
-    out[2 * r] = Y0 / Zt;
-    out[2 * r + 1] = Y1 / Zt;
+            *(s8v*)(Qls + r * 136 + g * 8) =
+                *(const s8v*)(p.q2 + (size_t)(row0 + r) * DZ + g * 8);
+        }
+        __syncthreads();
+        s8v af[4];
+#pragma unroll
+        for (int ks = 0; ks < 4; ++ks)
+            af[ks] = *(const s8v*)(Qls + (wave * 16 + lm) * 136 + ks * 32 + lq * 8);
+        float z[4] = {0.f, 0.f, 0.f, 0.f};
+        float y0[4] = {0.f, 0.f, 0.f, 0.f};
+        float y1[4] = {0.f, 0.f, 0.f, 0.f};
+        for (int t = 0; t < 8; ++t) {
+            int col0 = chunk * 512 + t * 64;
+            __syncthreads();
+#pragma unroll
+            for (int l = 0; l < 4; ++l) {
+                int id = l * 256 + tid;
+                int r = id >> 4, g = id & 15;
+                *(s8v*)(Kls + r * 136 + g * 8) =
+                    *(const s8v*)(p.kk + (size_t)(col0 + r) * 256 + 128 + g * 8);
+            }
+            if (tid < 128) Vls[tid] = p.v2b[col0 * 2 + tid];
+            __syncthreads();
+            f32x4 acc[4];
+#pragma unroll
+            for (int nt = 0; nt < 4; ++nt) acc[nt] = zero4;
+#pragma unroll
+            for (int nt = 0; nt < 4; ++nt)
+#pragma unroll
+                for (int ks = 0; ks < 4; ++ks) {
+                    s8v bf = *(const s8v*)(Kls + (nt * 16 + lm) * 136 + ks * 32 + lq * 8);
+                    acc[nt] = __builtin_amdgcn_mfma_f32_16x16x32_bf16(af[ks], bf, acc[nt], 0, 0, 0);
+                }
+            float v0[4], v1[4];
+#pragma unroll
+            for (int nt = 0; nt < 4; ++nt) {
+                v0[nt] = Vls[(nt * 16 + lm) * 2];
+                v1[nt] = Vls[(nt * 16 + lm) * 2 + 1];
+            }
+#pragma unroll
+            for (int i = 0; i < 4; ++i) {
+                float e0 = __expf(acc[0][i]), e1 = __expf(acc[1][i]);
+                float e2 = __expf(acc[2][i]), e3 = __expf(acc[3][i]);
+                float pz = e0 + e1 + e2 + e3;
+                float py0 = e0 * v0[0] + e1 * v0[1] + e2 * v0[2] + e3 * v0[3];
+                float py1 = e0 * v1[0] + e1 * v1[1] + e2 * v1[2] + e3 * v1[3];
+#pragma unroll
+                for (int msk = 1; msk < 16; msk <<= 1) {
+                    pz  += __shfl_xor(pz, msk, 64);
+                    py0 += __shfl_xor(py0, msk, 64);
+                    py1 += __shfl_xor(py1, msk, 64);
+                }
+                z[i] += pz; y0[i] += py0; y1[i] += py1;
+            }
+        }
+        if (lm == 0) {
+#pragma unroll
+            for (int i = 0; i < 4; ++i) {
+                int r = row0 + wave * 16 + lq * 4 + i;
+                float* pp = p.part2 + ((size_t)r * 8 + chunk) * 4;
+                pp[0] = z[i]; pp[1] = y0[i]; pp[2] = y1[i];
+            }
+        }
+    }
+    gbar(p.bar, 256u * 9);
+
+    {
+        int r = bid * 256 + tid;
+        if (r < N2) {
+            const float* pp = p.part2 + (size_t)r * 32;
+            float Zt = 0.f, Y0 = 0.f, Y1 = 0.f;
+#pragma unroll
+            for (int c = 0; c < 8; ++c) {
+                Zt += pp[c * 4]; Y0 += pp[c * 4 + 1]; Y1 += pp[c * 4 + 2];
+            }
+            p.out[2 * r] = Y0 / Zt;
+            p.out[2 * r + 1] = Y1 / Zt;
+        }
+    }
 }
 
 extern "C" void kernel_launch(void* const* d_in, const int* in_sizes, int n_in,
                               void* d_out, int out_size, void* d_ws, size_t ws_size,
                               hipStream_t stream) {
-    const float* lm_X = (const float*)d_in[0];
-    const float* lm_Y = (const float*)d_in[1];
-    const float* tg_X = (const float*)d_in[2];
-    const float* lm_delay = (const float*)d_in[4];
-    const float* tg_delay = (const float*)d_in[5];
-    const float* aq_w = (const float*)d_in[6];
-    const float* aq_b = (const float*)d_in[7];
-    const float* ak_w = (const float*)d_in[8];
-    const float* ak_b = (const float*)d_in[9];
-    const float* w1_w = (const float*)d_in[10];
-    const float* w1_b = (const float*)d_in[11];
-    const float* w2_w = (const float*)d_in[12];
-    const float* w2_b = (const float*)d_in[13];
-    const float* pq_w = (const float*)d_in[14];
-    const float* pq_b = (const float*)d_in[15];
-    const float* pk_w = (const float*)d_in[16];
-    const float* pk_b = (const float*)d_in[17];
-    const float* pv_w = (const float*)d_in[18];
-    const float* pv_b = (const float*)d_in[19];
-    const float* g1 = (const float*)d_in[20];
-    const float* g2 = (const float*)d_in[21];
-    const float* g3 = (const float*)d_in[22];
-    const float* al = (const float*)d_in[23];
-    const float* be = (const float*)d_in[24];
-
-    float* out = (float*)d_out;
-    float* outF = out + (size_t)N2 * 2;
+    P prm;
+    prm.lmX = (const float*)d_in[0];
+    prm.lmY = (const float*)d_in[1];
+    prm.tgX = (const float*)d_in[2];
+    prm.lmd = (const float*)d_in[4];
+    prm.tgd = (const float*)d_in[5];
+    prm.aqw = (const float*)d_in[6];
+    prm.aqb = (const float*)d_in[7];
+    prm.akw = (const float*)d_in[8];
+    prm.akb = (const float*)d_in[9];
+    prm.w1w = (const float*)d_in[10];
+    prm.w1b = (const float*)d_in[11];
+    prm.w2w = (const float*)d_in[12];
+    prm.w2b = (const float*)d_in[13];
+    prm.pqw = (const float*)d_in[14];
+    prm.pqb = (const float*)d_in[15];
+    prm.pkw = (const float*)d_in[16];
+    prm.pkb = (const float*)d_in[17];
+    prm.pvw = (const float*)d_in[18];
+    prm.pvb = (const float*)d_in[19];
+    prm.g1 = (const float*)d_in[20];
+    prm.g2 = (const float*)d_in[21];
+    prm.g3 = (const float*)d_in[22];
+    prm.al = (const float*)d_in[23];
+    prm.be = (const float*)d_in[24];
+
+    prm.out = (float*)d_out;
+    prm.outF = prm.out + (size_t)N2 * 2;
 
     char* base = (char*)d_ws;
     size_t off = 0;
     auto allocF = [&](size_t n) -> float* {
-        float* p = (float*)(base + off);
+        float* q = (float*)(base + off);
         off += (n * 4 + 255) / 256 * 256;
-        return p;
+        return q;
     };
     auto allocS = [&](size_t n) -> short* {
-        short* p = (short*)(base + off);
+        short* q = (short*)(base + off);
         off += (n * 2 + 255) / 256 * 256;
-        return p;
+        return q;
     };
 
-    short* E        = allocS((size_t)N2 * N1);
-    float* appart   = allocF((size_t)SPLITS * N2 * APN);
-    short* lmFTb    = allocS((size_t)APN * N1);
-    short* lmXb     = allocS((size_t)N1 * PD);
-    short* tgXb     = allocS((size_t)N2 * PD);
-    short* qb_b     = allocS((size_t)N2 * DZ);
-    short* kk       = allocS((size_t)N1 * 256);
-    short* q2_b     = allocS((size_t)N2 * DZ);
-    short* tgp0b    = allocS((size_t)N2 * PD2P);
-    short* tgp1b    = allocS((size_t)N2 * PD2P);
-    short* finalFb  = allocS((size_t)N2 * FDP);
-    short* aqwb     = allocS((size_t)DZ * PD);
-    short* wkkb     = allocS((size_t)256 * 256);
-    short* pqwb     = allocS((size_t)DZ * FDP);
-    short* w1wb     = allocS((size_t)PD2 * PD2P);
-    short* w2wb     = allocS((size_t)PD2 * PD2P);
-    float* v2b      = allocF((size_t)N1 * 2);
-    float* part2    = allocF((size_t)N2 * 32);
-    float* Zbuf     = allocF(N2);
-    float* biasKK   = allocF(256);
-    float* router0  = allocF(PD2);
-    float* routerp0 = allocF(PD2);
-    float* router1  = allocF(PD2);
-    float* dscore   = allocF(N1);
-    float* rou0     = allocF(N2);
-    float* rou1     = allocF(N2);
-
-    const float INV_TEMP = 0.08838834764831845f;
-
-    hipLaunchKernelGGL(cvt_all, dim3((S9 + 255) / 256), dim3(256), 0, stream,
-                       lm_X, lm_Y, tg_X, aq_w, ak_w, pk_w, pq_w, w1_w, w2_w,
-                       lm_delay, tg_delay, g1, g2, g3, al, be, pv_w, pv_b, ak_b, pk_b,
-                       lmXb, tgXb, aqwb, wkkb, pqwb, w1wb, w2wb, lmFTb,
-                       dscore, rou0, rou1, v2b, Zbuf, finalFb, tgp1b, biasKK, outF);
-    hipLaunchKernelGGL(router_kernel, dim3(PD2), dim3(256), 0, stream,
-                       lmFTb, dscore, router0, routerp0);
-    hipLaunchKernelGGL(router1_kernel, dim3(1), dim3(256), 0, stream,
-                       routerp0, w1_w, w1_b, router1);
-
-    hipLaunchKernelGGL(proj_gemm, dim3(4, 64), dim3(256), 0, stream,
-                       lmXb, wkkb, biasKK, kk, N1, 256, PD, 256, 1.f);
-    hipLaunchKernelGGL(proj_gemm, dim3(2, 32), dim3(256), 0, stream,
-                       tgXb, aqwb, aq_b, qb_b, N2, DZ, PD, DZ, INV_TEMP);
-    hipLaunchKernelGGL(scores_e, dim3(32, 16), dim3(256), 0, stream, qb_b, kk, E, Zbuf);
-    hipLaunchKernelGGL(ap_gemm, dim3(SPLITS, N2 / 128), dim3(256), 0, stream,
-                       E, Zbuf, lmFTb, appart);
-    hipLaunchKernelGGL(fix_tgp0, dim3(N2), dim3(256), 0, stream,
-                       appart, tg_X, rou0, router0, tgp0b);
-    hipLaunchKernelGGL(w_gemm, dim3(5, 32), dim3(256), 0, stream,
-                       tgp0b, w1wb, w1_b, outF + 256, finalFb + 256, rou1, router1, tgp1b);
-    hipLaunchKernelGGL(w_gemm, dim3(5, 32), dim3(256), 0, stream,
-                       tgp1b, w2wb, w2_b, outF + 514, finalFb + 514,
-                       nullptr, nullptr, nullptr);
-    hipLaunchKernelGGL(proj_gemm, dim3(2, 32), dim3(256), 0, stream,
-                       finalFb, pqwb, pq_b, q2_b, N2, DZ, FDP, DZ, INV_TEMP);
-    hipLaunchKernelGGL(attn2_flash, dim3(8, N2 / 64), dim3(256), 0, stream,
-                       q2_b, kk, v2b, part2);
-    hipLaunchKernelGGL(attn2_combine, dim3((N2 + 255) / 256), dim3(256), 0, stream,
-                       part2, out);
+    prm.E       = allocS((size_t)N2 * N1);
+    prm.appart  = allocF((size_t)SPLITS * N2 * APN);
+    prm.lmFTb   = allocS((size_t)APN * N1);
+    prm.qb      = allocS((size_t)N2 * DZ);
+    prm.kk      = allocS((size_t)N1 * 256);
+    prm.q2      = allocS((size_t)N2 * DZ);
+    prm.tgp0b   = allocS((size_t)N2 * PD2P);
+    prm.tgp1b   = allocS((size_t)N2 * PD2P);
+    prm.finalFb = allocS((size_t)N2 * FDP);
+    prm.w1wb    = allocS((size_t)PD2 * PD2P);
+    prm.w2wb    = allocS((size_t)PD2 * PD2P);
+    prm.pqwb    = allocS((size_t)DZ * FDP);
+    prm.v2b     = allocF((size_t)N1 * 2);
+    prm.part2   = allocF((size_t)N2 * 32);
+    prm.Z       = allocF(N2);
+    prm.router0 = allocF(PD2);
+    prm.routerp0= allocF(PD2);
+    prm.router1 = allocF(PD2);
+    prm.dscore  = allocF(N1);
+    prm.rou0    = allocF(N2);
+    prm.rou1    = allocF(N2);
+    prm.bar     = (unsigned*)allocF(64);
+
+    hipMemsetAsync(prm.bar, 0, 256, stream);
+    hipLaunchKernelGGL(mega, dim3(256), dim3(256), 0, stream, prm);
 }
```

Result: slower. 438.6 us (+73.9%).
